# Performance work log

Measured on AMD Instinct MI355X. Metric: run time of the kernel, lower is better.

The kernel has to match this reference:

```python
import jax, jax.numpy as jnp
import numpy as np

Q, C, T = 256, 128, 128
L = Q + C + T            # 512
D = 1024                 # d_model
H = 8                    # heads
DK = D // H              # 128 = self_attn.d_k
F = 3                    # num_latent_relations
R = 50                   # num_relation_kinds = len(relations2id)
FF = 4 * D               # feed-forward hidden
DEFAULT_QQ_ID = 0        # relations2id['q:q-default']
EPS = 1e-5


def setup_inputs():
    key = jax.random.key(0)
    ks = jax.random.split(key, 40)
    s = 0.02
    def nrm(k, shape, scale=s):
        return jax.random.normal(k, shape, jnp.float32) * scale
    inp = {
        'x': jax.random.normal(ks[0], (1, L, D), jnp.float32),
        'qc_relation': jax.random.uniform(ks[1], (Q, C, F), jnp.float32),
        'cq_relation': jax.random.uniform(ks[2], (C, Q, F), jnp.float32),
        'qt_relation': jax.random.uniform(ks[3], (Q, T, F), jnp.float32),
        'tq_relation': jax.random.uniform(ks[4], (T, Q, F), jnp.float32),
        'ct_relation': jax.random.randint(ks[5], (C + T, C + T), 0, R, jnp.int32),
        'predefined_relation': jax.random.randint(ks[6], (L, L), 0, R, jnp.int32),
        'mask': jnp.ones((1, L, L), jnp.int32),
        # relation embedding tables
        'rel_k_emb': nrm(ks[7], (R, DK)), 'rel_v_emb': nrm(ks[8], (R, DK)),
        'lqc_k': nrm(ks[9], (F, DK)), 'lqc_v': nrm(ks[10], (F, DK)),
        'lcq_k': nrm(ks[11], (F, DK)), 'lcq_v': nrm(ks[12], (F, DK)),
        'lqt_k': nrm(ks[13], (F, DK)), 'lqt_v': nrm(ks[14], (F, DK)),
        'ltq_k': nrm(ks[15], (F, DK)), 'ltq_v': nrm(ks[16], (F, DK)),
        # attention projections (torch Linear: y = x @ W.T + b)
        'Wq': nrm(ks[17], (D, D)), 'bq': jnp.zeros((D,), jnp.float32),
        'Wk': nrm(ks[18], (D, D)), 'bk': jnp.zeros((D,), jnp.float32),
        'Wv': nrm(ks[19], (D, D)), 'bv': jnp.zeros((D,), jnp.float32),
        'Wo': nrm(ks[20], (D, D)), 'bo': jnp.zeros((D,), jnp.float32),
        # layer norms
        'ln1_g': jnp.ones((D,), jnp.float32), 'ln1_b': jnp.zeros((D,), jnp.float32),
        'ln2_g': jnp.ones((D,), jnp.float32), 'ln2_b': jnp.zeros((D,), jnp.float32),
        # FFN
        'W1': nrm(ks[21], (FF, D)), 'b1': jnp.zeros((FF,), jnp.float32),
        'W2': nrm(ks[22], (D, FF)), 'b2': jnp.zeros((D,), jnp.float32),
    }
    return inp


def layer_norm(x, g, b):
    m = jnp.mean(x, -1, keepdims=True)
    v = jnp.mean((x - m) ** 2, -1, keepdims=True)
    return (x - m) * jax.lax.rsqrt(v + EPS) * g + b


def build_latent_relation(ct, qc, cq, qt, tq, emb, lqc, lcq, lqt, ltq):
    # qq block: every entry is the default-qq embedding row
    qq = jnp.broadcast_to(emb[DEFAULT_QQ_ID], (Q, Q, DK))
    qc_e = jnp.einsum('qcf,fd->qcd', qc, lqc)
    cq_e = jnp.einsum('cqf,fd->cqd', cq, lcq)
    qt_e = jnp.einsum('qtf,fd->qtd', qt, lqt)
    tq_e = jnp.einsum('tqf,fd->tqd', tq, ltq)
    ct_e = emb[ct]                                      # [(c+t),(c+t),DK]
    top = jnp.concatenate([qq, qc_e, qt_e], axis=1)      # [Q, L, DK]
    bot = jnp.concatenate([jnp.concatenate([cq_e, tq_e], 0), ct_e], axis=1)  # [C+T, L, DK]
    return jnp.concatenate([top, bot], axis=0)           # [L, L, DK]


def relation_attention(x, rel_k, rel_v, mask, Wq, bq, Wk, bk, Wv, bv, Wo, bo):
    B = x.shape[0]
    def proj(W, b):
        return (x @ W.T + b).reshape(B, L, H, DK).transpose(0, 2, 1, 3)  # [B,H,L,DK]
    q, k, v = proj(Wq, bq), proj(Wk, bk), proj(Wv, bv)
    scores = (jnp.einsum('bhid,bhjd->bhij', q, k)
              + jnp.einsum('bhid,ijd->bhij', q, rel_k)) / jnp.sqrt(jnp.float32(DK))
    scores = jnp.where(mask[:, None] == 0, jnp.float32(-1e9), scores)
    p = jax.nn.softmax(scores, axis=-1)
    o = (jnp.einsum('bhij,bhjd->bhid', p, v)
         + jnp.einsum('bhij,ijd->bhid', p, rel_v))
    o = o.transpose(0, 2, 1, 3).reshape(B, L, D)
    return o @ Wo.T + bo


def reference(x, qc_relation, cq_relation, qt_relation, tq_relation,
              ct_relation, predefined_relation, mask,
              rel_k_emb, rel_v_emb, lqc_k, lqc_v, lcq_k, lcq_v,
              lqt_k, lqt_v, ltq_k, ltq_v,
              Wq, bq, Wk, bk, Wv, bv, Wo, bo,
              ln1_g, ln1_b, ln2_g, ln2_b, W1, b1, W2, b2):
    # latent relation build + combine with predefined lookup
    rel_k = (rel_k_emb[predefined_relation]
             + build_latent_relation(ct_relation, qc_relation, cq_relation,
                                     qt_relation, tq_relation,
                                     rel_k_emb, lqc_k, lcq_k, lqt_k, ltq_k))
    rel_v = (rel_v_emb[predefined_relation]
             + build_latent_relation(ct_relation, qc_relation, cq_relation,
                                     qt_relation, tq_relation,
                                     rel_v_emb, lqc_v, lcq_v, lqt_v, ltq_v))
    # sublayer 0: pre-norm relation-biased self attention (dropout=0)
    h = x + relation_attention(layer_norm(x, ln1_g, ln1_b), rel_k, rel_v, mask,
                               Wq, bq, Wk, bk, Wv, bv, Wo, bo)
    # sublayer 1: pre-norm FFN
    y = layer_norm(h, ln2_g, ln2_b)
    ffn = jax.nn.relu(y @ W1.T + b1) @ W2.T + b2
    return h + ffn
```

## Files before the change

kernel.cpp:

```cpp
#include <hip/hip_runtime.h>
#include <hip/hip_bf16.h>

#define LL 512
#define DD 1024
#define HH 8
#define DKK 128
#define QQ 256
#define CCC 128
#define TTT 128
#define RR 50
#define FFF 4096

typedef __attribute__((ext_vector_type(8))) short short8;
typedef __attribute__((ext_vector_type(4))) float float4v;

__device__ __forceinline__ unsigned short f2bu(float f) {
  __hip_bfloat16 h = __float2bfloat16(f);
  unsigned short u; __builtin_memcpy(&u, &h, 2); return u;
}
__device__ __forceinline__ float b2f(unsigned short u) {
  unsigned int v = ((unsigned int)u) << 16;
  float f; __builtin_memcpy(&f, &v, 4); return f;
}

__device__ __forceinline__ void lds_barrier() {
  __builtin_amdgcn_sched_barrier(0);
  __builtin_amdgcn_s_waitcnt(0xC07F);
  __builtin_amdgcn_s_barrier();
  __builtin_amdgcn_sched_barrier(0);
}

#define GLOADSET(R0,R1,S0,S1,itv) {                                          \
  int k0v = (itv) << 6;                                                      \
  R0 = *(const int4*)(Az + (size_t)(bm + r)*lda + k0v + gc*8);               \
  R1 = *(const int4*)(Az + (size_t)(bm + 32 + r)*lda + k0v + gc*8);          \
  S0 = *(const int4*)(Bz + (size_t)(bn + r)*ldb + k0v + gc*8);               \
  if constexpr (NB > 1) {                                                    \
    S1 = *(const int4*)(Bz + (size_t)(bn + 32 + r)*ldb + k0v + gc*8); } }

#define STORESET(basep,R0,R1,S0,S1) {                                        \
  char* bse = (basep);                                                       \
  *(int4*)(bse + r*128 + sl*16) = R0;                                        \
  *(int4*)(bse + (32 + r)*128 + sl*16) = R1;                                 \
  *(int4*)(bse + ABYTES + r*128 + sl*16) = S0;                               \
  if constexpr (NB > 1) {                                                    \
    *(int4*)(bse + ABYTES + (32 + r)*128 + sl*16) = S1; } }

__global__ __launch_bounds__(256) void conv_kernel(
    const float* __restrict__ Wq, const float* __restrict__ Wk,
    const float* __restrict__ Wv, const float* __restrict__ Wo,
    const float* __restrict__ W1, const float* __restrict__ W2,
    const float* __restrict__ bq, const float* __restrict__ bk,
    const float* __restrict__ bv,
    unsigned short* __restrict__ wqkv, unsigned short* __restrict__ wo,
    unsigned short* __restrict__ w1, unsigned short* __restrict__ w2,
    float* __restrict__ bqkv)
{
  int g = blockIdx.x * 256 + threadIdx.x;
  const float* src; unsigned short* dst; int off;
  if (g < 262144)        { src = Wq; dst = wqkv;           off = g; }
  else if (g < 524288)   { src = Wk; dst = wqkv + 1048576; off = g - 262144; }
  else if (g < 786432)   { src = Wv; dst = wqkv + 2097152; off = g - 524288; }
  else if (g < 1048576)  { src = Wo; dst = wo;             off = g - 786432; }
  else if (g < 2097152)  { src = W1; dst = w1;             off = g - 1048576; }
  else if (g < 3145728)  { src = W2; dst = w2;             off = g - 2097152; }
  else if (g < 3145728 + 768) {
    int q = g - 3145728;
    const float* s = (q < 256) ? bq : (q < 512) ? bk : bv;
    ((float4*)bqkv)[q] = ((const float4*)s)[q & 255];
    return;
  } else return;
  float4 v = ((const float4*)src)[off];
  ushort4 o4;
  o4.x = f2bu(v.x); o4.y = f2bu(v.y); o4.z = f2bu(v.z); o4.w = f2bu(v.w);
  ((ushort4*)dst)[off] = o4;
}

__global__ __launch_bounds__(256) void ln_bf16_kernel(const float* __restrict__ x,
    const float* __restrict__ g, const float* __restrict__ b,
    unsigned short* __restrict__ y)
{
  int row = blockIdx.x, t = threadIdx.x;
  const float4 xv = ((const float4*)(x + row*DD))[t];
  float s  = xv.x+xv.y+xv.z+xv.w;
  float ss = xv.x*xv.x+xv.y*xv.y+xv.z*xv.z+xv.w*xv.w;
  __shared__ float rs[256], rss[256];
  rs[t]=s; rss[t]=ss; __syncthreads();
  for (int st=128; st>0; st>>=1){ if (t<st){ rs[t]+=rs[t+st]; rss[t]+=rss[t+st]; } __syncthreads(); }
  float mean = rs[0] * (1.0f/DD);
  float var  = rss[0]*(1.0f/DD) - mean*mean;
  float inv  = rsqrtf(var + 1e-5f);
  float4 gv = ((const float4*)g)[t], bv = ((const float4*)b)[t];
  ushort4 ov;
  ov.x = f2bu((xv.x-mean)*inv*gv.x + bv.x);
  ov.y = f2bu((xv.y-mean)*inv*gv.y + bv.y);
  ov.z = f2bu((xv.z-mean)*inv*gv.z + bv.z);
  ov.w = f2bu((xv.w-mean)*inv*gv.w + bv.w);
  ((ushort4*)(y + row*DD))[t] = ov;
}

__global__ __launch_bounds__(256) void addbias_kernel(float* __restrict__ out,
                                                      const float* __restrict__ b2)
{
  int g = blockIdx.x*256 + threadIdx.x;
  out[g] += b2[g & (DD-1)];
}

template<int BN, int ZK, int OUT_BF16, int RELU, int HAS_SRC, int HAS_BIAS>
__global__ __launch_bounds__(256) void gemm_pl(
    const unsigned short* __restrict__ A, int lda, size_t sAz,
    const unsigned short* __restrict__ B, int ldb, size_t sBz,
    const float* __restrict__ bias,
    const float* __restrict__ src, int ldsrc, size_t sSz,
    void* __restrict__ Cv, int ldc, size_t sCz,
    int K)
{
  constexpr int BM = 64;
  constexpr int WM = 32, WN = BN/2, FM = 2, FN = WN/16;
  constexpr int NB = BN/32;
  constexpr int ABYTES = BM*128, TILE = ABYTES + BN*128;
  __shared__ char lds[2*TILE];
  int t = threadIdx.x, w = t >> 6, l = t & 63;
  size_t z = blockIdx.z;
  const unsigned short* Az = A + z*sAz;
  const unsigned short* Bz = B + z*sBz;
  int bm = blockIdx.y*BM, bn = blockIdx.x*BN;
  int wm = (w>>1)*WM, wn = (w&1)*WN;

  float4v acc[FM][FN];
  #pragma unroll
  for (int m=0;m<FM;++m)
    #pragma unroll
    for (int n=0;n<FN;++n) acc[m][n] = (float4v){0.f,0.f,0.f,0.f};

  int r = t >> 3, sl = t & 7;
  int gc = sl ^ (r & 7);
  int quad = l >> 4, lrow = l & 15;
  const int nit = K >> 6;

  int4 a0, a1, b0, b1;
  int4 c0, c1, d0, d1;

  auto compute = [&](const char* base) {
    const char* ab = base;
    const char* bb = base + ABYTES;
    #pragma unroll
    for (int step=0; step<2; ++step) {
      int c = step*4 + quad;
      short8 af[FM], bf[FN];
      #pragma unroll
      for (int m=0;m<FM;++m) {
        int Rw = wm + m*16 + lrow;
        af[m] = *(const short8*)(ab + Rw*128 + ((c ^ (Rw & 7))*16));
      }
      #pragma unroll
      for (int n=0;n<FN;++n) {
        int Rw = wn + n*16 + lrow;
        bf[n] = *(const short8*)(bb + Rw*128 + ((c ^ (Rw & 7))*16));
      }
      #pragma unroll
      for (int m=0;m<FM;++m)
        #pragma unroll
        for (int n=0;n<FN;++n)
          acc[m][n] = __builtin_amdgcn_mfma_f32_16x16x32_bf16(af[m], bf[n], acc[m][n], 0, 0, 0);
    }
  };

  GLOADSET(a0,a1,b0,b1, 0);
  GLOADSET(c0,c1,d0,d1, 1);
  for (int it = 0; it < nit; it += 2) {
    STORESET(lds, a0,a1,b0,b1);
    if (it + 2 < nit) GLOADSET(a0,a1,b0,b1, it+2);
    lds_barrier();
    compute(lds);
    STORESET(lds + TILE, c0,c1,d0,d1);
    if (it + 3 < nit) GLOADSET(c0,c1,d0,d1, it+3);
    lds_barrier();
    compute(lds + TILE);
  }

  #pragma unroll
  for (int m=0;m<FM;++m)
    #pragma unroll
    for (int n=0;n<FN;++n)
      #pragma unroll
      for (int rg=0;rg<4;++rg) {
        int row = bm + wm + m*16 + quad*4 + rg;
        int col = bn + wn + n*16 + lrow;
        float vv = acc[m][n][rg];
        if (ZK) {
          atomicAdd(&((float*)Cv)[(size_t)row*ldc + col], vv);
        } else {
          if (HAS_BIAS) vv += bias[col];
          if (HAS_SRC)  vv += src[z*sSz + (size_t)row*ldsrc + col];
          if (RELU) vv = fmaxf(vv, 0.f);
          if (OUT_BF16) ((unsigned short*)Cv)[z*sCz + (size_t)row*ldc + col] = f2bu(vv);
          else          ((float*)Cv)[z*sCz + (size_t)row*ldc + col] = vv;
        }
      }
}

__global__ __launch_bounds__(256) void gemm_qkv_pl(
    const unsigned short* __restrict__ A, const unsigned short* __restrict__ B,
    const float* __restrict__ bqkv,
    unsigned short* __restrict__ Qh, unsigned short* __restrict__ Kh,
    unsigned short* __restrict__ Vt)
{
  constexpr int BN = 64;
  constexpr int WM = 32, WN = 32, FM = 2, FN = 2;
  constexpr int NB = 2;
  constexpr int ABYTES = 64*128, TILE = ABYTES + BN*128;
  __shared__ char lds[2*TILE];
  int t = threadIdx.x, w = t >> 6, l = t & 63;
  int bm = blockIdx.y*64, bn = blockIdx.x*BN;
  int wm = (w>>1)*WM, wn = (w&1)*WN;
  const int lda = DD, ldb = DD, nit = DD >> 6;
  const unsigned short* Az = A;
  const unsigned short* Bz = B;

  float4v acc[FM][FN];
  #pragma unroll
  for (int m=0;m<FM;++m)
    #pragma unroll
    for (int n=0;n<FN;++n) acc[m][n] = (float4v){0.f,0.f,0.f,0.f};

  int r = t >> 3, sl = t & 7;
  int gc = sl ^ (r & 7);
  int quad = l >> 4, lrow = l & 15;

  int4 a0, a1, b0, b1;
  int4 c0, c1, d0, d1;

  auto compute = [&](const char* base) {
    const char* ab = base;
    const char* bb = base + ABYTES;
    #pragma unroll
    for (int step=0; step<2; ++step) {
      int c = step*4 + quad;
      short8 af[FM], bf[FN];
      #pragma unroll
      for (int m=0;m<FM;++m) {
        int Rw = wm + m*16 + lrow;
        af[m] = *(const short8*)(ab + Rw*128 + ((c ^ (Rw & 7))*16));
      }
      #pragma unroll
      for (int n=0;n<FN;++n) {
        int Rw = wn + n*16 + lrow;
        bf[n] = *(const short8*)(bb + Rw*128 + ((c ^ (Rw & 7))*16));
      }
      #pragma unroll
      for (int m=0;m<FM;++m)
        #pragma unroll
        for (int n=0;n<FN;++n)
          acc[m][n] = __builtin_amdgcn_mfma_f32_16x16x32_bf16(af[m], bf[n], acc[m][n], 0, 0, 0);
    }
  };

  GLOADSET(a0,a1,b0,b1, 0);
  GLOADSET(c0,c1,d0,d1, 1);
  for (int it = 0; it < nit; it += 2) {
    STORESET(lds, a0,a1,b0,b1);
    if (it + 2 < nit) GLOADSET(a0,a1,b0,b1, it+2);
    lds_barrier();
    compute(lds);
    STORESET(lds + TILE, c0,c1,d0,d1);
    if (it + 3 < nit) GLOADSET(c0,c1,d0,d1, it+3);
    lds_barrier();
    compute(lds + TILE);
  }

  #pragma unroll
  for (int m=0;m<FM;++m)
    #pragma unroll
    for (int n=0;n<FN;++n)
      #pragma unroll
      for (int rg=0;rg<4;++rg) {
        int row = bm + wm + m*16 + quad*4 + rg;
        int col = bn + wn + n*16 + lrow;
        float vv = acc[m][n][rg] + bqkv[col];
        int part = col >> 10, hh = (col >> 7) & 7, d = col & 127;
        unsigned short o = f2bu(vv);
        if (part == 0)      Qh[((size_t)hh*LL + row)*DKK + d] = o;
        else if (part == 1) Kh[((size_t)hh*LL + row)*DKK + d] = o;
        else                Vt[((size_t)hh*DKK + d)*LL + row] = o;
      }
}

__global__ __launch_bounds__(64) void qtab_kernel(const unsigned short* __restrict__ Qh,
    const float* __restrict__ embk,
    const float* __restrict__ lqc, const float* __restrict__ lqt,
    const float* __restrict__ lcq, const float* __restrict__ ltq,
    float* __restrict__ qe, float* __restrict__ ql)
{
  int i = blockIdx.x, h = blockIdx.y, t = threadIdx.x;
  __shared__ float qrow[128];
  const unsigned short* qp = Qh + ((size_t)h*LL + i)*DKK;
  qrow[t] = b2f(qp[t]); qrow[t+64] = b2f(qp[t+64]);
  __syncthreads();
  if (t < RR) {
    float s = 0.f;
    #pragma unroll 8
    for (int d=0; d<128; ++d) s += qrow[d]*embk[t*128+d];
    qe[(i*HH+h)*RR + t] = s;
  } else if (t < RR + 12) {
    int u = t - RR;
    int tb = u/3, f = u - tb*3;
    const float* tab = (tb==0) ? lqc : (tb==1) ? lqt : (tb==2) ? lcq : ltq;
    const float* tr = tab + f*128;
    float s = 0.f;
    #pragma unroll 8
    for (int d=0; d<128; ++d) s += qrow[d]*tr[d];
    ql[((tb*LL + i)*HH + h)*3 + f] = s;
  }
}

__global__ __launch_bounds__(512) void softmax_kernel(
    float* __restrict__ S,
    const float* __restrict__ qe, const float* __restrict__ ql,
    const float* __restrict__ qcr, const float* __restrict__ cqr,
    const float* __restrict__ qtr, const float* __restrict__ tqr,
    const int* __restrict__ ct,   const int* __restrict__ pred,
    const int* __restrict__ mask)
{
  int i = blockIdx.x, h = blockIdx.y, j = threadIdx.x;
  __shared__ float qerow[52];
  __shared__ float red[512];
  if (j < RR) qerow[j] = qe[(i*HH+h)*RR + j];
  __syncthreads();

  float lq1[3] = {0,0,0}, lq2[3] = {0,0,0};
  if (i < QQ) {
    #pragma unroll
    for (int f=0; f<3; ++f) {
      lq1[f] = ql[((0*LL + i)*HH + h)*3 + f];
      lq2[f] = ql[((1*LL + i)*HH + h)*3 + f];
    }
  } else if (i < QQ+CCC) {
    #pragma unroll
    for (int f=0; f<3; ++f) lq1[f] = ql[((2*LL + i)*HH + h)*3 + f];
  } else {
    #pragma unroll
    for (int f=0; f<3; ++f) lq1[f] = ql[((3*LL + i)*HH + h)*3 + f];
  }

  float s = S[((size_t)h*LL + i)*LL + j];
  s += qerow[pred[i*LL + j]];
  if (i < QQ) {
    if (j < QQ) s += qerow[0];
    else if (j < QQ+CCC) { const float* r = qcr + (i*CCC + (j-QQ))*3;
      s += r[0]*lq1[0]+r[1]*lq1[1]+r[2]*lq1[2]; }
    else { const float* r = qtr + (i*TTT + (j-QQ-CCC))*3;
      s += r[0]*lq2[0]+r[1]*lq2[1]+r[2]*lq2[2]; }
  } else {
    if (j < QQ) {
      const float* r = (i < QQ+CCC) ? cqr + ((i-QQ)*QQ + j)*3
                                    : tqr + ((i-QQ-CCC)*QQ + j)*3;
      s += r[0]*lq1[0]+r[1]*lq1[1]+r[2]*lq1[2];
    } else {
      s += qerow[ct[(i-QQ)*(CCC+TTT) + (j-QQ)]];
    }
  }
  s *= 0.08838834764831845f;
  if (mask[i*LL + j] == 0) s = -1e9f;

  red[j] = s; __syncthreads();
  for (int st=256; st>0; st>>=1){ if (j<st) red[j]=fmaxf(red[j],red[j+st]); __syncthreads(); }
  float mx = red[0]; __syncthreads();
  float e = __expf(s - mx);
  red[j] = e; __syncthreads();
  for (int st=256; st>0; st>>=1){ if (j<st) red[j]+=red[j+st]; __syncthreads(); }
  float inv = 1.0f/red[0];
  ((unsigned short*)S)[((size_t)h*LL + i)*1024 + j] = f2bu(e*inv);
}

__global__ __launch_bounds__(256) void pw_kernel(
    const unsigned short* __restrict__ P,
    const float* __restrict__ embv,
    const float* __restrict__ lqc_v, const float* __restrict__ lcq_v,
    const float* __restrict__ lqt_v, const float* __restrict__ ltq_v,
    const float* __restrict__ qcr,  const float* __restrict__ cqr,
    const float* __restrict__ qtr,  const float* __restrict__ tqr,
    const int* __restrict__ ct,    const int* __restrict__ pred,
    float* __restrict__ o2)
{
  int i = blockIdx.x, t = threadIdx.x;
  __shared__ float pw8[8][56];
  __shared__ float pf1s[24], pf2s[24];
  __shared__ int predrow[512];
  __shared__ int ctrow[256];
  for (int k=t; k<8*56; k+=256) ((float*)pw8)[k] = 0.f;
  if (t < 24) { pf1s[t]=0.f; pf2s[t]=0.f; }
  for (int k=t; k<512; k+=256) predrow[k] = pred[i*LL + k];
  if (i >= QQ) { if (t < 256) ctrow[t] = ct[(i-QQ)*(CCC+TTT) + t]; }
  __syncthreads();

  int h = t >> 5, lane = t & 31;
  float qq = 0.f, l1[3] = {0,0,0}, l2[3] = {0,0,0};
  const unsigned short* Prow = P + ((size_t)h*LL + i)*1024;
  for (int jj = 0; jj < 16; ++jj) {
    int j = lane + jj*32;
    float p = b2f(Prow[j]);
    atomicAdd(&pw8[h][predrow[j]], p);
    if (i < QQ) {
      if (j < QQ) qq += p;
      else if (j < QQ+CCC) { const float* r = qcr + (i*CCC + (j-QQ))*3;
        l1[0]+=p*r[0]; l1[1]+=p*r[1]; l1[2]+=p*r[2]; }
      else { const float* r = qtr + (i*TTT + (j-QQ-CCC))*3;
        l2[0]+=p*r[0]; l2[1]+=p*r[1]; l2[2]+=p*r[2]; }
    } else {
      if (j < QQ) {
        const float* r = (i < QQ+CCC) ? cqr + ((i-QQ)*QQ + j)*3
                                      : tqr + ((i-QQ-CCC)*QQ + j)*3;
        l1[0]+=p*r[0]; l1[1]+=p*r[1]; l1[2]+=p*r[2];
      } else {
        atomicAdd(&pw8[h][ctrow[j-QQ]], p);
      }
    }
  }
  if (i < QQ) atomicAdd(&pw8[h][0], qq);
  atomicAdd(&pf1s[h*3+0], l1[0]); atomicAdd(&pf1s[h*3+1], l1[1]); atomicAdd(&pf1s[h*3+2], l1[2]);
  atomicAdd(&pf2s[h*3+0], l2[0]); atomicAdd(&pf2s[h*3+1], l2[1]); atomicAdd(&pf2s[h*3+2], l2[2]);
  __syncthreads();

  const float* tab1; const float* tab2 = nullptr;
  if (i < QQ)          { tab1 = lqc_v; tab2 = lqt_v; }
  else if (i < QQ+CCC) { tab1 = lcq_v; }
  else                 { tab1 = ltq_v; }

  for (int o = t; o < 1024; o += 256) {
    int h2 = o >> 7, d = o & 127;
    float acc = 0.f;
    #pragma unroll 5
    for (int r = 0; r < RR; ++r) acc += pw8[h2][r]*embv[r*128 + d];
    acc += pf1s[h2*3+0]*tab1[d] + pf1s[h2*3+1]*tab1[128+d] + pf1s[h2*3+2]*tab1[256+d];
    if (tab2) acc += pf2s[h2*3+0]*tab2[d] + pf2s[h2*3+1]*tab2[128+d] + pf2s[h2*3+2]*tab2[256+d];
    o2[((size_t)h2*LL + i)*DKK + d] = acc;
  }
}

extern "C" void kernel_launch(void* const* d_in, const int* in_sizes, int n_in,
                              void* d_out, int out_size, void* d_ws, size_t ws_size,
                              hipStream_t stream)
{
  const float* x    = (const float*)d_in[0];
  const float* qcr  = (const float*)d_in[1];
  const float* cqr  = (const float*)d_in[2];
  const float* qtr  = (const float*)d_in[3];
  const float* tqr  = (const float*)d_in[4];
  const int*   ct   = (const int*)d_in[5];
  const int*   pred = (const int*)d_in[6];
  const int*   mask = (const int*)d_in[7];
  const float* embk = (const float*)d_in[8];
  const float* embv = (const float*)d_in[9];
  const float* lqc_k = (const float*)d_in[10];
  const float* lqc_v = (const float*)d_in[11];
  const float* lcq_k = (const float*)d_in[12];
  const float* lcq_v = (const float*)d_in[13];
  const float* lqt_k = (const float*)d_in[14];
  const float* lqt_v = (const float*)d_in[15];
  const float* ltq_k = (const float*)d_in[16];
  const float* ltq_v = (const float*)d_in[17];
  const float* Wq = (const float*)d_in[18]; const float* bq = (const float*)d_in[19];
  const float* Wk = (const float*)d_in[20]; const float* bk = (const float*)d_in[21];
  const float* Wv = (const float*)d_in[22]; const float* bv = (const float*)d_in[23];
  const float* Wo = (const float*)d_in[24]; const float* bo = (const float*)d_in[25];
  const float* ln1_g = (const float*)d_in[26]; const float* ln1_b = (const float*)d_in[27];
  const float* ln2_g = (const float*)d_in[28]; const float* ln2_b = (const float*)d_in[29];
  const float* W1 = (const float*)d_in[30]; const float* b1 = (const float*)d_in[31];
  const float* W2 = (const float*)d_in[32]; const float* b2 = (const float*)d_in[33];
  float* out = (float*)d_out;

  float* wsf = (float*)d_ws;
  float* S    = wsf;
  float* o2   = S + (size_t)HH*LL*LL;
  float* qe   = o2 + (size_t)HH*LL*DKK;
  float* ql   = qe + LL*HH*RR;
  float* bqkv = ql + 4*LL*HH*3;
  unsigned short* ub = (unsigned short*)(bqkv + 3072);
  unsigned short* ybuf_b = ub;
  unsigned short* obuf_b = ybuf_b + LL*DD;
  unsigned short* Qh     = obuf_b + LL*DD;
  unsigned short* Kh     = Qh + LL*DD;
  unsigned short* Vt     = Kh + LL*DD;
  unsigned short* wqkv_b = Vt + LL*DD;
  unsigned short* wo_b   = wqkv_b + (size_t)3*DD*DD;
  unsigned short* w1_b   = wo_b + (size_t)DD*DD;
  unsigned short* w2_b   = w1_b + (size_t)FFF*DD;
  unsigned short* PS     = (unsigned short*)S;
  unsigned short* hidden = (unsigned short*)S;

  conv_kernel<<<(3145728 + 768 + 255)/256, 256, 0, stream>>>(
      Wq, Wk, Wv, Wo, W1, W2, bq, bk, bv, wqkv_b, wo_b, w1_b, w2_b, bqkv);
  ln_bf16_kernel<<<LL, 256, 0, stream>>>(x, ln1_g, ln1_b, ybuf_b);
  gemm_qkv_pl<<<dim3(48, 8), 256, 0, stream>>>(ybuf_b, wqkv_b, bqkv, Qh, Kh, Vt);
  qtab_kernel<<<dim3(LL, HH), 64, 0, stream>>>(Qh, embk, lqc_k, lqt_k, lcq_k, ltq_k, qe, ql);
  gemm_pl<64,0,0,0,0,0><<<dim3(8, 8, 8), 256, 0, stream>>>(
      Qh, DKK, (size_t)LL*DKK, Kh, DKK, (size_t)LL*DKK,
      nullptr, nullptr, 0, 0, S, LL, (size_t)LL*LL, DKK);
  softmax_kernel<<<dim3(LL, HH), 512, 0, stream>>>(S, qe, ql, qcr, cqr, qtr, tqr,
                                                   ct, pred, mask);
  pw_kernel<<<LL, 256, 0, stream>>>(PS, embv, lqc_v, lcq_v, lqt_v, ltq_v,
                                    qcr, cqr, qtr, tqr, ct, pred, o2);
  gemm_pl<32,0,1,0,1,0><<<dim3(4, 8, 8), 256, 0, stream>>>(
      PS, 1024, (size_t)LL*1024, Vt, LL, (size_t)DKK*LL,
      nullptr, o2, DKK, (size_t)LL*DKK, obuf_b, DD, (size_t)DKK, LL);
  gemm_pl<32,0,0,0,1,1><<<dim3(32, 8, 1), 256, 0, stream>>>(
      obuf_b, DD, 0, wo_b, DD, 0, bo, x, DD, 0, out, DD, 0, DD);
  ln_bf16_kernel<<<LL, 256, 0, stream>>>(out, ln2_g, ln2_b, ybuf_b);
  gemm_pl<64,0,1,1,0,1><<<dim3(64, 8, 1), 256, 0, stream>>>(
      ybuf_b, DD, 0, w1_b, DD, 0, b1, nullptr, 0, 0, hidden, FFF, 0, DD);
  addbias_kernel<<<(LL*DD)/256, 256, 0, stream>>>(out, b2);
  gemm_pl<64,1,0,0,0,0><<<dim3(16, 8, 4), 256, 0, stream>>>(
      hidden, FFF, (size_t)1024, w2_b, FFF, (size_t)1024,
      nullptr, nullptr, 0, 0, out, DD, 0, 1024);
}
```

Baseline: 271.7 us.

## Fuse fp32-to-bf16 weight conversion into GEMM tile loads

Removes the separate weight conversion kernel and its bf16 weight buffers. The QKV, output-projection and FFN GEMMs now load fp32 weight tiles directly and convert them to bf16 in registers before storing to LDS. Biases are read straight from the original arrays. This avoids a full read-write pass over all weights. In exchange each GEMM block reads twice the bytes per weight tile, and weights are re-read by every M-tile block, which raises load traffic and register pressure.

```diff
diff --git a/kernel.cpp b/kernel.cpp
--- a/kernel.cpp
+++ b/kernel.cpp
@@ -22,6 +22,14 @@
   unsigned int v = ((unsigned int)u) << 16;
   float f; __builtin_memcpy(&f, &v, 4); return f;
 }
+__device__ __forceinline__ int4 cvt8(float4 x, float4 y) {
+  int4 o;
+  o.x = (int)f2bu(x.x) | ((int)f2bu(x.y) << 16);
+  o.y = (int)f2bu(x.z) | ((int)f2bu(x.w) << 16);
+  o.z = (int)f2bu(y.x) | ((int)f2bu(y.y) << 16);
+  o.w = (int)f2bu(y.z) | ((int)f2bu(y.w) << 16);
+  return o;
+}
 
 __device__ __forceinline__ void lds_barrier() {
   __builtin_amdgcn_sched_barrier(0);
@@ -30,51 +38,32 @@
   __builtin_amdgcn_sched_barrier(0);
 }
 
-#define GLOADSET(R0,R1,S0,S1,itv) {                                          \
-  int k0v = (itv) << 6;                                                      \
-  R0 = *(const int4*)(Az + (size_t)(bm + r)*lda + k0v + gc*8);               \
-  R1 = *(const int4*)(Az + (size_t)(bm + 32 + r)*lda + k0v + gc*8);          \
-  S0 = *(const int4*)(Bz + (size_t)(bn + r)*ldb + k0v + gc*8);               \
-  if constexpr (NB > 1) {                                                    \
-    S1 = *(const int4*)(Bz + (size_t)(bn + 32 + r)*ldb + k0v + gc*8); } }
-
-#define STORESET(basep,R0,R1,S0,S1) {                                        \
-  char* bse = (basep);                                                       \
-  *(int4*)(bse + r*128 + sl*16) = R0;                                        \
-  *(int4*)(bse + (32 + r)*128 + sl*16) = R1;                                 \
-  *(int4*)(bse + ABYTES + r*128 + sl*16) = S0;                               \
-  if constexpr (NB > 1) {                                                    \
-    *(int4*)(bse + ABYTES + (32 + r)*128 + sl*16) = S1; } }
-
-__global__ __launch_bounds__(256) void conv_kernel(
-    const float* __restrict__ Wq, const float* __restrict__ Wk,
-    const float* __restrict__ Wv, const float* __restrict__ Wo,
-    const float* __restrict__ W1, const float* __restrict__ W2,
-    const float* __restrict__ bq, const float* __restrict__ bk,
-    const float* __restrict__ bv,
-    unsigned short* __restrict__ wqkv, unsigned short* __restrict__ wo,
-    unsigned short* __restrict__ w1, unsigned short* __restrict__ w2,
-    float* __restrict__ bqkv)
-{
-  int g = blockIdx.x * 256 + threadIdx.x;
-  const float* src; unsigned short* dst; int off;
-  if (g < 262144)        { src = Wq; dst = wqkv;           off = g; }
-  else if (g < 524288)   { src = Wk; dst = wqkv + 1048576; off = g - 262144; }
-  else if (g < 786432)   { src = Wv; dst = wqkv + 2097152; off = g - 524288; }
-  else if (g < 1048576)  { src = Wo; dst = wo;             off = g - 786432; }
-  else if (g < 2097152)  { src = W1; dst = w1;             off = g - 1048576; }
-  else if (g < 3145728)  { src = W2; dst = w2;             off = g - 2097152; }
-  else if (g < 3145728 + 768) {
-    int q = g - 3145728;
-    const float* s = (q < 256) ? bq : (q < 512) ? bk : bv;
-    ((float4*)bqkv)[q] = ((const float4*)s)[q & 255];
-    return;
-  } else return;
-  float4 v = ((const float4*)src)[off];
-  ushort4 o4;
-  o4.x = f2bu(v.x); o4.y = f2bu(v.y); o4.z = f2bu(v.z); o4.w = f2bu(v.w);
-  ((ushort4*)dst)[off] = o4;
-}
+#define LOADSET(A0,A1,B0,B1,F0,F1,F2,F3,itv) { int k0v = (itv) << 6;          \
+  A0 = *(const int4*)(Az + (size_t)(bm + r)*lda + k0v + gc*8);                \
+  A1 = *(const int4*)(Az + (size_t)(bm + 32 + r)*lda + k0v + gc*8);           \
+  if constexpr (!CONVB) {                                                     \
+    B0 = *(const int4*)(Bz16 + (size_t)(bnb + r)*ldb + k0v + gc*8);           \
+    if constexpr (NB > 1)                                                     \
+      B1 = *(const int4*)(Bz16 + (size_t)(bnb + 32 + r)*ldb + k0v + gc*8);    \
+  } else {                                                                    \
+    F0 = *(const float4*)(Bz32 + (size_t)(bnb + r)*ldb + k0v + gc*8);         \
+    F1 = *(const float4*)(Bz32 + (size_t)(bnb + r)*ldb + k0v + gc*8 + 4);     \
+    if constexpr (NB > 1) {                                                   \
+      F2 = *(const float4*)(Bz32 + (size_t)(bnb + 32 + r)*ldb + k0v + gc*8);  \
+      F3 = *(const float4*)(Bz32 + (size_t)(bnb + 32 + r)*ldb + k0v + gc*8 + 4); } } }
+
+#define STORESET2(basep,A0,A1,B0,B1,F0,F1,F2,F3) {                            \
+  char* bse = (basep);                                                        \
+  *(int4*)(bse + r*128 + sl*16) = A0;                                         \
+  *(int4*)(bse + (32 + r)*128 + sl*16) = A1;                                  \
+  if constexpr (!CONVB) {                                                     \
+    *(int4*)(bse + ABYTES + r*128 + sl*16) = B0;                              \
+    if constexpr (NB > 1)                                                     \
+      *(int4*)(bse + ABYTES + (32 + r)*128 + sl*16) = B1;                     \
+  } else {                                                                    \
+    *(int4*)(bse + ABYTES + r*128 + sl*16) = cvt8(F0, F1);                    \
+    if constexpr (NB > 1)                                                     \
+      *(int4*)(bse + ABYTES + (32 + r)*128 + sl*16) = cvt8(F2, F3); } }
 
 __global__ __launch_bounds__(256) void ln_bf16_kernel(const float* __restrict__ x,
     const float* __restrict__ g, const float* __restrict__ b,
@@ -106,10 +95,10 @@
   out[g] += b2[g & (DD-1)];
 }
 
-template<int BN, int ZK, int OUT_BF16, int RELU, int HAS_SRC, int HAS_BIAS>
+template<int BN, int CONVB, int ZK, int OUT_BF16, int RELU, int HAS_SRC, int HAS_BIAS>
 __global__ __launch_bounds__(256) void gemm_pl(
     const unsigned short* __restrict__ A, int lda, size_t sAz,
-    const unsigned short* __restrict__ B, int ldb, size_t sBz,
+    const void* __restrict__ Bv, int ldb, size_t sBz,
     const float* __restrict__ bias,
     const float* __restrict__ src, int ldsrc, size_t sSz,
     void* __restrict__ Cv, int ldc, size_t sCz,
@@ -123,8 +112,10 @@
   int t = threadIdx.x, w = t >> 6, l = t & 63;
   size_t z = blockIdx.z;
   const unsigned short* Az = A + z*sAz;
-  const unsigned short* Bz = B + z*sBz;
+  const unsigned short* Bz16 = (const unsigned short*)Bv + (CONVB ? 0 : z*sBz);
+  const float*          Bz32 = (const float*)Bv + (CONVB ? z*sBz : 0);
   int bm = blockIdx.y*BM, bn = blockIdx.x*BN;
+  int bnb = bn;
   int wm = (w>>1)*WM, wn = (w&1)*WN;
 
   float4v acc[FM][FN];
@@ -138,8 +129,8 @@
   int quad = l >> 4, lrow = l & 15;
   const int nit = K >> 6;
 
-  int4 a0, a1, b0, b1;
-  int4 c0, c1, d0, d1;
+  int4 pa0, pa1, pb0, pb1;  float4 pf0, pf1, pf2, pf3;
+  int4 qa0, qa1, qb0, qb1;  float4 qf0, qf1, qf2, qf3;
 
   auto compute = [&](const char* base) {
     const char* ab = base;
@@ -166,15 +157,15 @@
     }
   };
 
-  GLOADSET(a0,a1,b0,b1, 0);
-  GLOADSET(c0,c1,d0,d1, 1);
+  LOADSET(pa0,pa1,pb0,pb1,pf0,pf1,pf2,pf3, 0);
+  LOADSET(qa0,qa1,qb0,qb1,qf0,qf1,qf2,qf3, 1);
   for (int it = 0; it < nit; it += 2) {
-    STORESET(lds, a0,a1,b0,b1);
-    if (it + 2 < nit) GLOADSET(a0,a1,b0,b1, it+2);
+    STORESET2(lds, pa0,pa1,pb0,pb1,pf0,pf1,pf2,pf3);
+    if (it + 2 < nit) LOADSET(pa0,pa1,pb0,pb1,pf0,pf1,pf2,pf3, it+2);
     lds_barrier();
     compute(lds);
-    STORESET(lds + TILE, c0,c1,d0,d1);
-    if (it + 3 < nit) GLOADSET(c0,c1,d0,d1, it+3);
+    STORESET2(lds + TILE, qa0,qa1,qb0,qb1,qf0,qf1,qf2,qf3);
+    if (it + 3 < nit) LOADSET(qa0,qa1,qb0,qb1,qf0,qf1,qf2,qf3, it+3);
     lds_barrier();
     compute(lds + TILE);
   }
@@ -201,12 +192,15 @@
 }
 
 __global__ __launch_bounds__(256) void gemm_qkv_pl(
-    const unsigned short* __restrict__ A, const unsigned short* __restrict__ B,
-    const float* __restrict__ bqkv,
+    const unsigned short* __restrict__ A,
+    const float* __restrict__ Wq, const float* __restrict__ Wk,
+    const float* __restrict__ Wv,
+    const float* __restrict__ bq, const float* __restrict__ bk,
+    const float* __restrict__ bv,
     unsigned short* __restrict__ Qh, unsigned short* __restrict__ Kh,
     unsigned short* __restrict__ Vt)
 {
-  constexpr int BN = 64;
+  constexpr int BN = 64, CONVB = 1;
   constexpr int WM = 32, WN = 32, FM = 2, FN = 2;
   constexpr int NB = 2;
   constexpr int ABYTES = 64*128, TILE = ABYTES + BN*128;
@@ -216,7 +210,10 @@
   int wm = (w>>1)*WM, wn = (w&1)*WN;
   const int lda = DD, ldb = DD, nit = DD >> 6;
   const unsigned short* Az = A;
-  const unsigned short* Bz = B;
+  int part0 = bn >> 10;
+  const float* Bz32 = (part0==0 ? Wq : part0==1 ? Wk : Wv) + (size_t)(bn & 1023)*DD;
+  const unsigned short* Bz16 = nullptr; (void)Bz16;
+  int bnb = 0;
 
   float4v acc[FM][FN];
   #pragma unroll
@@ -228,8 +225,8 @@
   int gc = sl ^ (r & 7);
   int quad = l >> 4, lrow = l & 15;
 
-  int4 a0, a1, b0, b1;
-  int4 c0, c1, d0, d1;
+  int4 pa0, pa1, pb0, pb1;  float4 pf0, pf1, pf2, pf3;
+  int4 qa0, qa1, qb0, qb1;  float4 qf0, qf1, qf2, qf3;
 
   auto compute = [&](const char* base) {
     const char* ab = base;
@@ -256,15 +253,15 @@
     }
   };
 
-  GLOADSET(a0,a1,b0,b1, 0);
-  GLOADSET(c0,c1,d0,d1, 1);
+  LOADSET(pa0,pa1,pb0,pb1,pf0,pf1,pf2,pf3, 0);
+  LOADSET(qa0,qa1,qb0,qb1,qf0,qf1,qf2,qf3, 1);
   for (int it = 0; it < nit; it += 2) {
-    STORESET(lds, a0,a1,b0,b1);
-    if (it + 2 < nit) GLOADSET(a0,a1,b0,b1, it+2);
+    STORESET2(lds, pa0,pa1,pb0,pb1,pf0,pf1,pf2,pf3);
+    if (it + 2 < nit) LOADSET(pa0,pa1,pb0,pb1,pf0,pf1,pf2,pf3, it+2);
     lds_barrier();
     compute(lds);
-    STORESET(lds + TILE, c0,c1,d0,d1);
-    if (it + 3 < nit) GLOADSET(c0,c1,d0,d1, it+3);
+    STORESET2(lds + TILE, qa0,qa1,qb0,qb1,qf0,qf1,qf2,qf3);
+    if (it + 3 < nit) LOADSET(qa0,qa1,qb0,qb1,qf0,qf1,qf2,qf3, it+3);
     lds_barrier();
     compute(lds + TILE);
   }
@@ -277,8 +274,9 @@
       for (int rg=0;rg<4;++rg) {
         int row = bm + wm + m*16 + quad*4 + rg;
         int col = bn + wn + n*16 + lrow;
-        float vv = acc[m][n][rg] + bqkv[col];
         int part = col >> 10, hh = (col >> 7) & 7, d = col & 127;
+        const float* bp = (part==0) ? bq : (part==1) ? bk : bv;
+        float vv = acc[m][n][rg] + bp[col & 1023];
         unsigned short o = f2bu(vv);
         if (part == 0)      Qh[((size_t)hh*LL + row)*DKK + d] = o;
         else if (part == 1) Kh[((size_t)hh*LL + row)*DKK + d] = o;
@@ -475,42 +473,36 @@
   float* o2   = S + (size_t)HH*LL*LL;
   float* qe   = o2 + (size_t)HH*LL*DKK;
   float* ql   = qe + LL*HH*RR;
-  float* bqkv = ql + 4*LL*HH*3;
-  unsigned short* ub = (unsigned short*)(bqkv + 3072);
+  unsigned short* ub = (unsigned short*)(ql + 4*LL*HH*3);
   unsigned short* ybuf_b = ub;
   unsigned short* obuf_b = ybuf_b + LL*DD;
   unsigned short* Qh     = obuf_b + LL*DD;
   unsigned short* Kh     = Qh + LL*DD;
   unsigned short* Vt     = Kh + LL*DD;
-  unsigned short* wqkv_b = Vt + LL*DD;
-  unsigned short* wo_b   = wqkv_b + (size_t)3*DD*DD;
-  unsigned short* w1_b   = wo_b + (size_t)DD*DD;
-  unsigned short* w2_b   = w1_b + (size_t)FFF*DD;
   unsigned short* PS     = (unsigned short*)S;
   unsigned short* hidden = (unsigned short*)S;
 
-  conv_kernel<<<(3145728 + 768 + 255)/256, 256, 0, stream>>>(
-      Wq, Wk, Wv, Wo, W1, W2, bq, bk, bv, wqkv_b, wo_b, w1_b, w2_b, bqkv);
   ln_bf16_kernel<<<LL, 256, 0, stream>>>(x, ln1_g, ln1_b, ybuf_b);
-  gemm_qkv_pl<<<dim3(48, 8), 256, 0, stream>>>(ybuf_b, wqkv_b, bqkv, Qh, Kh, Vt);
+  gemm_qkv_pl<<<dim3(48, 8), 256, 0, stream>>>(ybuf_b, Wq, Wk, Wv, bq, bk, bv,
+                                               Qh, Kh, Vt);
   qtab_kernel<<<dim3(LL, HH), 64, 0, stream>>>(Qh, embk, lqc_k, lqt_k, lcq_k, ltq_k, qe, ql);
-  gemm_pl<64,0,0,0,0,0><<<dim3(8, 8, 8), 256, 0, stream>>>(
+  gemm_pl<64,0,0,0,0,0,0><<<dim3(8, 8, 8), 256, 0, stream>>>(
       Qh, DKK, (size_t)LL*DKK, Kh, DKK, (size_t)LL*DKK,
       nullptr, nullptr, 0, 0, S, LL, (size_t)LL*LL, DKK);
   softmax_kernel<<<dim3(LL, HH), 512, 0, stream>>>(S, qe, ql, qcr, cqr, qtr, tqr,
                                                    ct, pred, mask);
   pw_kernel<<<LL, 256, 0, stream>>>(PS, embv, lqc_v, lcq_v, lqt_v, ltq_v,
                                     qcr, cqr, qtr, tqr, ct, pred, o2);
-  gemm_pl<32,0,1,0,1,0><<<dim3(4, 8, 8), 256, 0, stream>>>(
+  gemm_pl<32,0,0,1,0,1,0><<<dim3(4, 8, 8), 256, 0, stream>>>(
       PS, 1024, (size_t)LL*1024, Vt, LL, (size_t)DKK*LL,
       nullptr, o2, DKK, (size_t)LL*DKK, obuf_b, DD, (size_t)DKK, LL);
-  gemm_pl<32,0,0,0,1,1><<<dim3(32, 8, 1), 256, 0, stream>>>(
-      obuf_b, DD, 0, wo_b, DD, 0, bo, x, DD, 0, out, DD, 0, DD);
+  gemm_pl<32,1,0,0,0,1,1><<<dim3(32, 8, 1), 256, 0, stream>>>(
+      obuf_b, DD, 0, Wo, DD, 0, bo, x, DD, 0, out, DD, 0, DD);
   ln_bf16_kernel<<<LL, 256, 0, stream>>>(out, ln2_g, ln2_b, ybuf_b);
-  gemm_pl<64,0,1,1,0,1><<<dim3(64, 8, 1), 256, 0, stream>>>(
-      ybuf_b, DD, 0, w1_b, DD, 0, b1, nullptr, 0, 0, hidden, FFF, 0, DD);
+  gemm_pl<64,1,0,1,1,0,1><<<dim3(64, 8, 1), 256, 0, stream>>>(
+      ybuf_b, DD, 0, W1, DD, 0, b1, nullptr, 0, 0, hidden, FFF, 0, DD);
   addbias_kernel<<<(LL*DD)/256, 256, 0, stream>>>(out, b2);
-  gemm_pl<64,1,0,0,0,0><<<dim3(16, 8, 4), 256, 0, stream>>>(
-      hidden, FFF, (size_t)1024, w2_b, FFF, (size_t)1024,
+  gemm_pl<64,1,1,0,0,0,0><<<dim3(16, 8, 4), 256, 0, stream>>>(
+      hidden, FFF, (size_t)1024, W2, FFF, (size_t)1024,
       nullptr, nullptr, 0, 0, out, DD, 0, 1024);
 }
```

Measured after the change: 273.8 us. Within noise of the previous version (+0.8%).
